# Performance work log

Measured on AMD Instinct MI355X. Metric: run time of the kernel, lower is better.

## Reference

```python
import jax, jax.numpy as jnp
import numpy as np
import math

B_, V_, D_, N_, H_, W_ = 4, 8, 64, 16, 32, 32
V_LIST = [0.0, 45.0, 90.0, 135.0, 180.0, 225.0, 270.0, 315.0]
GROUPS = 4
EPS = 1e-5


def _make_sample_coords():
    # Replicates F.affine_grid(align_corners=False) for fixed rotation matrices,
    # then maps normalized grid coords to input pixel coords as grid_sample does.
    xs = (np.arange(W_) + 0.5) * 2.0 / W_ - 1.0
    ys = (np.arange(H_) + 0.5) * 2.0 / H_ - 1.0
    X, Y = np.meshgrid(xs, ys)  # (H, W)
    ix_list, iy_list = [], []
    for w in V_LIST:
        a = math.radians(-w)
        c, s = math.cos(a), math.sin(a)
        gx = c * X - s * Y  # theta = [[c,-s,0],[s,c,0]]
        gy = s * X + c * Y
        ix_list.append((gx + 1.0) * W_ / 2.0 - 0.5)
        iy_list.append((gy + 1.0) * H_ / 2.0 - 0.5)
    return (jnp.asarray(np.stack(ix_list), jnp.float32),
            jnp.asarray(np.stack(iy_list), jnp.float32))

IX, IY = _make_sample_coords()  # each (V, H, W)


def _bilinear(sv, iy, ix):
    # sv: (B, D, N, H, W); iy, ix: (H, W) float sampling coords (pixel space)
    x0 = jnp.floor(ix)
    y0 = jnp.floor(iy)
    wx1 = ix - x0
    wy1 = iy - y0

    def corner(yc, xc, wgt):
        m = (yc >= 0) & (yc < H_) & (xc >= 0) & (xc < W_)  # zeros padding
        yi = jnp.clip(yc, 0, H_ - 1).astype(jnp.int32)
        xi = jnp.clip(xc, 0, W_ - 1).astype(jnp.int32)
        return sv[..., yi, xi] * jnp.where(m, wgt, 0.0)

    return (corner(y0, x0, (1.0 - wy1) * (1.0 - wx1))
            + corner(y0, x0 + 1.0, (1.0 - wy1) * wx1)
            + corner(y0 + 1.0, x0, wy1 * (1.0 - wx1))
            + corner(y0 + 1.0, x0 + 1.0, wy1 * wx1))

# vmap over the velocity axis V of s_prev and the per-velocity grids
_transport = jax.vmap(_bilinear, in_axes=(1, 0, 0), out_axes=1)


def _conv(x, w, b=None):
    y = jax.lax.conv_general_dilated(x, w, (1, 1), 'SAME',
                                     dimension_numbers=('NCHW', 'OIHW', 'NCHW'))
    if b is not None:
        y = y + b[None, :, None, None]
    return y


def _group_norm(x, w, b):
    Bn, D, H, W = x.shape
    xg = x.reshape(Bn, GROUPS, D // GROUPS, H, W)
    mu = xg.mean(axis=(2, 3, 4), keepdims=True)
    var = xg.var(axis=(2, 3, 4), keepdims=True)
    xn = ((xg - mu) * jax.lax.rsqrt(var + EPS)).reshape(Bn, D, H, W)
    return xn * w[None, :, None, None] + b[None, :, None, None]


def setup_inputs() -> dict:
    key = jax.random.key(0)
    ks = jax.random.split(key, 5)
    return {
        "u_t": jax.random.normal(ks[0], (B_, D_, H_, W_), jnp.float32),
        "s_prev": jax.random.normal(ks[1], (B_, V_, D_, N_, H_, W_), jnp.float32) * 0.1,
        "gn_w": jnp.ones((D_,), jnp.float32),
        "gn_b": jnp.zeros((D_,), jnp.float32),
        "conv_delta_w": jax.random.normal(ks[2], (D_, D_, 3, 3), jnp.float32) * 0.02,
        "conv_delta_b": jnp.zeros((D_,), jnp.float32),
        "conv_B_w": jax.random.normal(ks[3], (N_, D_, 3, 3), jnp.float32) * 0.02,
        "conv_C_w": jax.random.normal(ks[4], (N_, D_, 3, 3), jnp.float32) * 0.02,
        "log_A_real": jnp.full((D_, N_), math.log(0.5), jnp.float32),
        "D_param": jnp.ones((D_,), jnp.float32),
        "dt_bias": jnp.float32(math.log(math.e - 1.0)),
    }


def reference(u_t, s_prev, gn_w, gn_b, conv_delta_w, conv_delta_b,
              conv_B_w, conv_C_w, log_A_real, D_param, dt_bias):
    u_norm = _group_norm(u_t, gn_w, gn_b)
    delta = jax.nn.softplus(_conv(u_norm, conv_delta_w, conv_delta_b) + dt_bias)
    delta = jnp.clip(delta, 1e-4, 5.0)                               # (B,D,H,W)
    B_val = _conv(u_norm, conv_B_w)                                  # (B,N,H,W)
    C_val = _conv(u_norm, conv_C_w)                                  # (B,N,H,W)
    A = -jnp.exp(log_A_real)                                         # (D,N)
    A_bar = jnp.exp(delta[:, :, None] * A[None, :, :, None, None])   # (B,D,N,H,W)
    B_bar = delta[:, :, None] * B_val[:, None]                       # (B,D,N,H,W)
    s_trans = _transport(s_prev, IY, IX)                             # (B,V,D,N,H,W)
    s_new = A_bar[:, None] * s_trans + B_bar[:, None] * u_t[:, None, :, None]
    y_state = jnp.einsum('bvdnhw,bnhw->bvdhw', s_new, C_val)
    y_new = y_state + u_t[:, None] * D_param[None, None, :, None, None]
    return (y_new, s_new)
```

## Files before the change

### kernel.cpp

```cpp
#include <hip/hip_runtime.h>
#include <cmath>

#define FSQ 0.70710678118654752440f
__constant__ float CTAB[8] = {1.f,  FSQ, 0.f, -FSQ, -1.f, -FSQ, 0.f, FSQ};
__constant__ float STAB[8] = {0.f, -FSQ, -1.f, -FSQ,  0.f,  FSQ, 1.f, FSQ};

__global__ __launch_bounds__(1024) void gn_kernel(const float* __restrict__ u,
                                                  const float* __restrict__ gw,
                                                  const float* __restrict__ gb,
                                                  float* __restrict__ up)
{
    int blk = blockIdx.x;
    int b = blk >> 2, g = blk & 3;
    int t = threadIdx.x;
    const float* src = u + ((size_t)(b * 64 + g * 16) << 10);
    float sum = 0.f, sq = 0.f;
    #pragma unroll
    for (int r = 0; r < 16; ++r) {
        float v = src[t + (r << 10)];
        sum += v; sq += v * v;
    }
    #pragma unroll
    for (int ofs = 32; ofs > 0; ofs >>= 1) {
        sum += __shfl_down(sum, ofs);
        sq  += __shfl_down(sq, ofs);
    }
    __shared__ float red[16], red2[16];
    int wv = t >> 6;
    if ((t & 63) == 0) { red[wv] = sum; red2[wv] = sq; }
    __syncthreads();
    float s_tot = 0.f, q_tot = 0.f;
    #pragma unroll
    for (int k = 0; k < 16; ++k) { s_tot += red[k]; q_tot += red2[k]; }
    float mu  = s_tot * (1.f / 16384.f);
    float var = q_tot * (1.f / 16384.f) - mu * mu;
    float rs  = rsqrtf(var + 1e-5f);

    float* pb = up + (size_t)(b * 64 + g * 16) * 1156;
    for (int k = t; k < 16 * 132; k += 1024) {
        int pl = k / 132, c = k - pl * 132;
        int idx;
        if (c < 34)       idx = c;
        else if (c < 68)  idx = 33 * 34 + (c - 34);
        else if (c < 100) idx = (c - 68 + 1) * 34;
        else              idx = (c - 100 + 1) * 34 + 33;
        pb[pl * 1156 + idx] = 0.f;
    }
    int y = t >> 5, x = t & 31;
    #pragma unroll
    for (int r = 0; r < 16; ++r) {
        float val = (src[t + (r << 10)] - mu) * rs * gw[g * 16 + r] + gb[g * 16 + r];
        pb[r * 1156 + (y + 1) * 34 + (x + 1)] = val;
    }
}

__global__ __launch_bounds__(256) void conv_kernel(const float* __restrict__ up,
                                                   const float* __restrict__ wd,
                                                   const float* __restrict__ bd,
                                                   const float* __restrict__ wB,
                                                   const float* __restrict__ wC,
                                                   const float* __restrict__ dtb,
                                                   float* __restrict__ delta,
                                                   float* __restrict__ Bv,
                                                   float* __restrict__ Cv)
{
    __shared__ float sin_[64 * 204];
    int blk = blockIdx.x;
    int strip = blk & 7;
    int og = (blk >> 3) % 24;
    int b = blk / 192;
    int h0 = strip * 4;
    int t = threadIdx.x;

    const float* plane = up + (size_t)b * 73984;
    for (int idx = t; idx < 13056; idx += 256) {
        int ci = idx / 204;
        int rem = idx - ci * 204;
        sin_[idx] = plane[ci * 1156 + h0 * 34 + rem];
    }
    __syncthreads();

    int o0 = og * 4;
    const float* wsel;
    if (o0 < 64)      wsel = wd + (size_t)o0 * 576;
    else if (o0 < 80) wsel = wB + (size_t)(o0 - 64) * 576;
    else              wsel = wC + (size_t)(o0 - 80) * 576;

    int half = t >> 7;
    int px = t & 127;
    int r = px >> 5, c = px & 31;
    const float* base = sin_ + r * 34 + c;

    float acc0 = 0.f, acc1 = 0.f, acc2 = 0.f, acc3 = 0.f;
    int ci0 = half * 32;
    for (int ci = ci0; ci < ci0 + 32; ++ci) {
        const float* pp = base + ci * 204;
        const float* wp = wsel + ci * 9;
        #pragma unroll
        for (int dy = 0; dy < 3; ++dy)
            #pragma unroll
            for (int dx = 0; dx < 3; ++dx) {
                float v = pp[dy * 34 + dx];
                int wi = dy * 3 + dx;
                acc0 += v * wp[wi];
                acc1 += v * wp[576 + wi];
                acc2 += v * wp[1152 + wi];
                acc3 += v * wp[1728 + wi];
            }
    }
    __syncthreads();
    float4* red4 = (float4*)sin_;
    red4[t] = make_float4(acc0, acc1, acc2, acc3);
    __syncthreads();
    if (t < 128) {
        float4 a = red4[t], bq = red4[t + 128];
        float s0 = a.x + bq.x, s1 = a.y + bq.y, s2 = a.z + bq.z, s3 = a.w + bq.w;
        float s[4] = {s0, s1, s2, s3};
        int pidx = (h0 + r) * 32 + c;
        if (o0 < 64) {
            #pragma unroll
            for (int k = 0; k < 4; ++k) {
                float x = s[k] + bd[o0 + k] + dtb[0];
                float sp = (x > 20.f) ? x : log1pf(expf(x));
                sp = fminf(fmaxf(sp, 1e-4f), 5.f);
                delta[((size_t)(b * 64 + o0 + k) << 10) + pidx] = sp;
            }
        } else if (o0 < 80) {
            #pragma unroll
            for (int k = 0; k < 4; ++k)
                Bv[((size_t)(b * 16 + o0 - 64 + k) << 10) + pidx] = s[k];
        } else {
            #pragma unroll
            for (int k = 0; k < 4; ++k)
                Cv[((size_t)(b * 16 + o0 - 80 + k) << 10) + pidx] = s[k];
        }
    }
}

__global__ __launch_bounds__(256) void fused_state_kernel(
    const float* __restrict__ s_prev, const float* __restrict__ u_t,
    const float* __restrict__ delta, const float* __restrict__ Bv,
    const float* __restrict__ Cv, const float* __restrict__ logA,
    const float* __restrict__ Dp, float* __restrict__ y_out,
    float* __restrict__ s_out)
{
    __shared__ float lds[4 * 1190];
    __shared__ float Ash[4];
    int blk = blockIdx.x;
    int cchunk = blk & 3;
    int d = (blk >> 2) & 63, v = (blk >> 8) & 7, b = blk >> 11;
    int t = threadIdx.x;

    if (t < 4) Ash[t] = -__expf(logA[d * 16 + cchunk * 4 + t]);
    for (int k = t; k < 528; k += 256) {
        int pl = k / 132, g = k - pl * 132;
        int idx;
        if (g < 34)       idx = g;
        else if (g < 68)  idx = 33 * 35 + (g - 34);
        else if (g < 100) idx = (g - 67) * 35;
        else              idx = (g - 99) * 35 + 33;
        lds[pl * 1190 + idx] = 0.f;
    }

    size_t so = (((size_t)((b * 8 + v) * 64 + d)) << 14) + ((size_t)cchunk << 12);
    const float4* src = (const float4*)(s_prev + so);
    #pragma unroll
    for (int k = 0; k < 4; ++k) {
        int q = t + (k << 8);
        float4 val = src[q];
        int lin = q << 2;
        int nn = lin >> 10, rem = lin & 1023;
        int di = nn * 1190 + ((rem >> 5) + 1) * 35 + (rem & 31) + 1;
        lds[di] = val.x; lds[di + 1] = val.y; lds[di + 2] = val.z; lds[di + 3] = val.w;
    }
    __syncthreads();

    const float cc = CTAB[v], ss = STAB[v];
    const float* dpl = delta + ((size_t)(b * 64 + d) << 10);
    const float* upl = u_t   + ((size_t)(b * 64 + d) << 10);
    const float* bvc = Bv + ((size_t)b << 14) + (cchunk << 12);
    const float* cvc = Cv + ((size_t)b << 14) + (cchunk << 12);
    float* soc = s_out + so;
    float* yo  = y_out + (((size_t)((b * 8 + v) * 64 + d)) << 10);
    float Dd = Dp[d];

    for (int i = 0; i < 4; ++i) {
        int p = t + (i << 8);
        int h = p >> 5, wpx = p & 31;
        float X = (wpx + 0.5f) * 0.0625f - 1.f;
        float Y = (h + 0.5f) * 0.0625f - 1.f;
        float gx = cc * X - ss * Y;
        float gy = ss * X + cc * Y;
        float ix = (gx + 1.f) * 16.f - 0.5f;
        float iy = (gy + 1.f) * 16.f - 0.5f;
        float fx0 = floorf(ix), fy0 = floorf(iy);
        float wx = ix - fx0, wy = iy - fy0;
        int x0 = (int)fx0, y0 = (int)fy0;
        float mx0 = (x0 >= 0 && x0 < 32) ? (1.f - wx) : 0.f;
        float mx1 = (x0 >= -1 && x0 < 31) ? wx : 0.f;
        float my0 = (y0 >= 0 && y0 < 32) ? (1.f - wy) : 0.f;
        float my1 = (y0 >= -1 && y0 < 31) ? wy : 0.f;
        float w00 = my0 * mx0, w01 = my0 * mx1;
        float w10 = my1 * mx0, w11 = my1 * mx1;
        int bx = min(max(x0, -1), 31), by = min(max(y0, -1), 31);
        int base = (by + 1) * 35 + (bx + 1);

        float dd = dpl[p], uv = upl[p];
        float du = dd * uv;
        float yacc = 0.f;
        #pragma unroll
        for (int nn = 0; nn < 4; ++nn) {
            int si = base + nn * 1190;
            float s00 = lds[si], s01 = lds[si + 1];
            float s10 = lds[si + 35], s11 = lds[si + 36];
            float bil = s00 * w00 + s01 * w01 + s10 * w10 + s11 * w11;
            float abar = __expf(dd * Ash[nn]);
            float bvv = bvc[(nn << 10) + p];
            float sn = abar * bil + du * bvv;
            soc[(nn << 10) + p] = sn;
            yacc += sn * cvc[(nn << 10) + p];
        }
        float val = yacc + (cchunk == 0 ? uv * Dd : 0.f);
        atomicAdd(yo + p, val);
    }
}

extern "C" void kernel_launch(void* const* d_in, const int* in_sizes, int n_in,
                              void* d_out, int out_size, void* d_ws, size_t ws_size,
                              hipStream_t stream)
{
    const float* u_t    = (const float*)d_in[0];
    const float* s_prev = (const float*)d_in[1];
    const float* gn_w   = (const float*)d_in[2];
    const float* gn_b   = (const float*)d_in[3];
    const float* wd     = (const float*)d_in[4];
    const float* bd     = (const float*)d_in[5];
    const float* wB     = (const float*)d_in[6];
    const float* wC     = (const float*)d_in[7];
    const float* logA   = (const float*)d_in[8];
    const float* Dp     = (const float*)d_in[9];
    const float* dtb    = (const float*)d_in[10];

    float* y_out = (float*)d_out;
    float* s_out = y_out + 2097152;

    float* up    = (float*)d_ws;
    float* delta = up + 295936;
    float* Bv    = delta + 262144;
    float* Cv    = Bv + 65536;

    hipMemsetAsync(y_out, 0, (size_t)2097152 * sizeof(float), stream);

    hipLaunchKernelGGL(gn_kernel, dim3(16), dim3(1024), 0, stream, u_t, gn_w, gn_b, up);
    hipLaunchKernelGGL(conv_kernel, dim3(768), dim3(256), 0, stream,
                       up, wd, bd, wB, wC, dtb, delta, Bv, Cv);
    hipLaunchKernelGGL(fused_state_kernel, dim3(8192), dim3(256), 0, stream,
                       s_prev, u_t, delta, Bv, Cv, logA, Dp, y_out, s_out);
}
```

Measured before the change: 303.1 us.

## Vectorize fused state kernel per-thread 4-pixel work and reorder block mapping

Each thread now handles four consecutive pixels, using float4 loads for delta, u, B and C and float4 nontemporal stores for the new state, replacing scalar strided accesses. The block index mapping is changed so the channel-chunk index is the slowest-varying dimension rather than the fastest, which alters which blocks run concurrently and contend on the same y atomics. This aims to cut memory instruction count and keep the large streaming state output from polluting cache, at the cost of more registers per thread and different atomic contention patterns.

```diff
diff --git a/kernel.cpp b/kernel.cpp
--- a/kernel.cpp
+++ b/kernel.cpp
@@ -4,6 +4,8 @@
 #define FSQ 0.70710678118654752440f
 __constant__ float CTAB[8] = {1.f,  FSQ, 0.f, -FSQ, -1.f, -FSQ, 0.f, FSQ};
 __constant__ float STAB[8] = {0.f, -FSQ, -1.f, -FSQ,  0.f,  FSQ, 1.f, FSQ};
+
+typedef float f4 __attribute__((ext_vector_type(4)));
 
 __global__ __launch_bounds__(1024) void gn_kernel(const float* __restrict__ u,
                                                   const float* __restrict__ gw,
@@ -147,8 +149,9 @@
     __shared__ float lds[4 * 1190];
     __shared__ float Ash[4];
     int blk = blockIdx.x;
-    int cchunk = blk & 3;
-    int d = (blk >> 2) & 63, v = (blk >> 8) & 7, b = blk >> 11;
+    int cchunk = blk >> 11;
+    int rest = blk & 2047;
+    int d = rest & 63, v = (rest >> 6) & 7, b = rest >> 9;
     int t = threadIdx.x;
 
     if (t < 4) Ash[t] = -__expf(logA[d * 16 + cchunk * 4 + t]);
@@ -176,21 +179,26 @@
     __syncthreads();
 
     const float cc = CTAB[v], ss = STAB[v];
-    const float* dpl = delta + ((size_t)(b * 64 + d) << 10);
-    const float* upl = u_t   + ((size_t)(b * 64 + d) << 10);
-    const float* bvc = Bv + ((size_t)b << 14) + (cchunk << 12);
-    const float* cvc = Cv + ((size_t)b << 14) + (cchunk << 12);
-    float* soc = s_out + so;
+    const f4* dpl4 = (const f4*)(delta + ((size_t)(b * 64 + d) << 10));
+    const f4* upl4 = (const f4*)(u_t   + ((size_t)(b * 64 + d) << 10));
+    const f4* bvc4 = (const f4*)(Bv + ((size_t)b << 14) + (cchunk << 12));
+    const f4* cvc4 = (const f4*)(Cv + ((size_t)b << 14) + (cchunk << 12));
+    f4* soc4   = (f4*)(s_out + so);
     float* yo  = y_out + (((size_t)((b * 8 + v) * 64 + d)) << 10);
     float Dd = Dp[d];
 
-    for (int i = 0; i < 4; ++i) {
-        int p = t + (i << 8);
-        int h = p >> 5, wpx = p & 31;
+    f4 dd4 = dpl4[t], uv4 = upl4[t];
+
+    int h = t >> 3;
+    float Yc = (h + 0.5f) * 0.0625f - 1.f;
+    float w00[4], w01[4], w10[4], w11[4], duv[4], yacc[4];
+    int tb[4];
+    #pragma unroll
+    for (int j = 0; j < 4; ++j) {
+        int wpx = ((t & 7) << 2) | j;
         float X = (wpx + 0.5f) * 0.0625f - 1.f;
-        float Y = (h + 0.5f) * 0.0625f - 1.f;
-        float gx = cc * X - ss * Y;
-        float gy = ss * X + cc * Y;
+        float gx = cc * X - ss * Yc;
+        float gy = ss * X + cc * Yc;
         float ix = (gx + 1.f) * 16.f - 0.5f;
         float iy = (gy + 1.f) * 16.f - 0.5f;
         float fx0 = floorf(ix), fy0 = floorf(iy);
@@ -200,28 +208,36 @@
         float mx1 = (x0 >= -1 && x0 < 31) ? wx : 0.f;
         float my0 = (y0 >= 0 && y0 < 32) ? (1.f - wy) : 0.f;
         float my1 = (y0 >= -1 && y0 < 31) ? wy : 0.f;
-        float w00 = my0 * mx0, w01 = my0 * mx1;
-        float w10 = my1 * mx0, w11 = my1 * mx1;
+        w00[j] = my0 * mx0; w01[j] = my0 * mx1;
+        w10[j] = my1 * mx0; w11[j] = my1 * mx1;
         int bx = min(max(x0, -1), 31), by = min(max(y0, -1), 31);
-        int base = (by + 1) * 35 + (bx + 1);
-
-        float dd = dpl[p], uv = upl[p];
-        float du = dd * uv;
-        float yacc = 0.f;
+        tb[j] = (by + 1) * 35 + (bx + 1);
+        duv[j] = dd4[j] * uv4[j];
+        yacc[j] = 0.f;
+    }
+
+    #pragma unroll
+    for (int nn = 0; nn < 4; ++nn) {
+        f4 B4 = bvc4[(nn << 8) + t];
+        f4 C4 = cvc4[(nn << 8) + t];
+        f4 sn4;
         #pragma unroll
-        for (int nn = 0; nn < 4; ++nn) {
-            int si = base + nn * 1190;
-            float s00 = lds[si], s01 = lds[si + 1];
-            float s10 = lds[si + 35], s11 = lds[si + 36];
-            float bil = s00 * w00 + s01 * w01 + s10 * w10 + s11 * w11;
-            float abar = __expf(dd * Ash[nn]);
-            float bvv = bvc[(nn << 10) + p];
-            float sn = abar * bil + du * bvv;
-            soc[(nn << 10) + p] = sn;
-            yacc += sn * cvc[(nn << 10) + p];
+        for (int j = 0; j < 4; ++j) {
+            int si = tb[j] + nn * 1190;
+            float bil = lds[si] * w00[j] + lds[si + 1] * w01[j]
+                      + lds[si + 35] * w10[j] + lds[si + 36] * w11[j];
+            float abar = __expf(dd4[j] * Ash[nn]);
+            float sn = abar * bil + duv[j] * B4[j];
+            sn4[j] = sn;
+            yacc[j] += sn * C4[j];
         }
-        float val = yacc + (cchunk == 0 ? uv * Dd : 0.f);
-        atomicAdd(yo + p, val);
+        __builtin_nontemporal_store(sn4, soc4 + (nn << 8) + t);
+    }
+
+    #pragma unroll
+    for (int j = 0; j < 4; ++j) {
+        float val = yacc[j] + (cchunk == 0 ? uv4[j] * Dd : 0.f);
+        atomicAdd(yo + (t << 2) + j, val);
     }
 }
 
```

Result: slower. 355.4 us (+17.3%).
